# Optimization experiments

Measured on AMD Instinct MI355X. Metric: run time of the kernel, lower is better.

## Reference

```python
import jax, jax.numpy as jnp
import numpy as np

N_NODES = 100000
N_EDGES = 1600000
X_DIM, E_DIM = 4, 39


def setup_inputs() -> dict:
    key = jax.random.key(0)
    ks = jax.random.split(key, 12)
    x = jax.random.normal(ks[0], (N_NODES, X_DIM), dtype=jnp.float32)
    edge_index = jax.random.randint(ks[1], (2, N_EDGES), 0, N_NODES, dtype=jnp.int64)
    edge_attr = jax.random.normal(ks[2], (N_EDGES, E_DIM), dtype=jnp.float32)
    def lin(k, fan_in, fan_out):
        kw, kb = jax.random.split(k)
        bound = 1.0 / np.sqrt(fan_in)
        W = jax.random.uniform(kw, (fan_in, fan_out), jnp.float32, -bound, bound)
        b = jax.random.uniform(kb, (fan_out,), jnp.float32, -bound, bound)
        return W, b
    W1, b1 = lin(ks[3], 43, 64)
    W2, b2 = lin(ks[4], 64, 128)
    W3, b3 = lin(ks[5], 132, 256)
    W4, b4 = lin(ks[6], 256, 256)
    return {"x": x, "edge_index": edge_index, "edge_attr": edge_attr,
            "W1": W1, "b1": b1, "W2": W2, "b2": b2,
            "W3": W3, "b3": b3, "W4": W4, "b4": b4}


def reference(x, edge_index, edge_attr, W1, b1, W2, b2, W3, b3, W4, b4):
    row, col = edge_index[0], edge_index[1]
    n = x.shape[0]
    # gather source-node features, concat edge attrs -> edge MLP
    h = jnp.concatenate([x[col], edge_attr], axis=1)            # [E, 43]
    h = jax.nn.relu(h @ W1 + b1)                                # [E, 64]
    h = jax.nn.relu(h @ W2 + b2)                                # [E, 128]
    # scatter_mean over edges grouped by destination node `row`
    s = jax.ops.segment_sum(h, row, num_segments=n)             # [N, 128]
    cnt = jax.ops.segment_sum(jnp.ones((row.shape[0],), h.dtype), row,
                              num_segments=n)                   # [N]
    mean = s / jnp.maximum(cnt, 1.0)[:, None]                   # 0 for empty segments
    # concat node features with aggregated messages -> node MLP
    o = jnp.concatenate([x, mean], axis=1)                      # [N, 132]
    o = jax.nn.relu(o @ W3 + b3)                                # [N, 256]
    o = jax.nn.relu(o @ W4 + b4)                                # [N, 256]
    return o
```

## Files before the change

kernel.cpp:

```cpp
#include <hip/hip_runtime.h>
#include <hip/hip_bf16.h>

#define NN 100000
#define NE 1600000
#define XD 4
#define ED 39
#define K1 43
#define H1 64
#define H2 128
#define H3 256
#define NBN 16
#define NCHUNK 98

typedef short bfrag8 __attribute__((ext_vector_type(8)));
typedef float facc4  __attribute__((ext_vector_type(4)));
typedef unsigned short u16x4 __attribute__((ext_vector_type(4)));

static __device__ __forceinline__ unsigned short f2bf(float f) {
    __hip_bfloat16 b = __float2bfloat16(f);
    union { __hip_bfloat16 b; unsigned short u; } v; v.b = b;
    return v.u;
}
static __device__ __forceinline__ float bf2f(unsigned short h) {
    union { unsigned int u; float f; } v; v.u = ((unsigned int)h) << 16;
    return v.f;
}

__global__ __launch_bounds__(256) void hist_kernel(const int* __restrict__ eidx,
                                                   int* __restrict__ cnt,
                                                   int* __restrict__ rank) {
    int e = blockIdx.x * 256 + threadIdx.x;
    if (e < NE) rank[e] = atomicAdd(&cnt[eidx[e]], 1);
}

__global__ __launch_bounds__(1024) void scan1_kernel(const int* __restrict__ cnt,
                                                     int* __restrict__ row_ptr,
                                                     int* __restrict__ chunkSum) {
    __shared__ int wsum[16];
    const int t = threadIdx.x, lane = t & 63, w = t >> 6;
    const int i = blockIdx.x * 1024 + t;
    int v = (i < NN) ? cnt[i] : 0;
    int s = v;
    #pragma unroll
    for (int d = 1; d < 64; d <<= 1) {
        int u = __shfl_up(s, d, 64);
        if (lane >= d) s += u;
    }
    if (lane == 63) wsum[w] = s;
    __syncthreads();
    if (w == 0 && lane < 16) {
        int e = wsum[lane];
        #pragma unroll
        for (int d = 1; d < 16; d <<= 1) {
            int u = __shfl_up(e, d, 64);
            if (lane >= d) e += u;
        }
        wsum[lane] = e;
    }
    __syncthreads();
    int woff = (w == 0) ? 0 : wsum[w - 1];
    if (i < NN) row_ptr[i + 1] = woff + s;
    if (t == 0) chunkSum[blockIdx.x] = wsum[15];
}

__global__ __launch_bounds__(64) void scan2_kernel(const int* __restrict__ chunkSum,
                                                   int* __restrict__ chunkOff) {
    const int lane = threadIdx.x;
    int a = (lane < NCHUNK) ? chunkSum[lane] : 0;
    int b = (lane + 64 < NCHUNK) ? chunkSum[lane + 64] : 0;
    int sa = a;
    #pragma unroll
    for (int d = 1; d < 64; d <<= 1) {
        int u = __shfl_up(sa, d, 64);
        if (lane >= d) sa += u;
    }
    int totA = __shfl(sa, 63, 64);
    int sb = b;
    #pragma unroll
    for (int d = 1; d < 64; d <<= 1) {
        int u = __shfl_up(sb, d, 64);
        if (lane >= d) sb += u;
    }
    sb += totA;
    if (lane < NCHUNK) chunkOff[lane] = sa - a;
    if (lane + 64 < NCHUNK) chunkOff[lane + 64] = sb - b;
}

__global__ __launch_bounds__(1024) void scan3_kernel(const int* __restrict__ chunkOff,
                                                     int* __restrict__ row_ptr) {
    const int i = blockIdx.x * 1024 + threadIdx.x;
    const int off = chunkOff[blockIdx.x];
    if (i < NN) row_ptr[i + 1] += off;
    if (i == 0) row_ptr[0] = 0;
}

__global__ __launch_bounds__(256) void build_kernel(const int* __restrict__ eidx,
                                                    const int* __restrict__ row_ptr,
                                                    const int* __restrict__ rank,
                                                    int* __restrict__ perm) {
    int e = blockIdx.x * 256 + threadIdx.x;
    if (e < NE) {
        int r = eidx[e];
        perm[row_ptr[r] + rank[e]] = e;
    }
}

__global__ __launch_bounds__(256) void prep_kernel(
    const float* __restrict__ W1, const float* __restrict__ W2,
    const float* __restrict__ W3, const float* __restrict__ W4,
    unsigned short* __restrict__ W1h, unsigned short* __restrict__ W1l,
    unsigned short* __restrict__ W2h, unsigned short* __restrict__ W2l,
    unsigned short* __restrict__ W3h, unsigned short* __restrict__ W3l,
    unsigned short* __restrict__ W4h, unsigned short* __restrict__ W4l)
{
    int i = blockIdx.x * 256 + threadIdx.x;
    if (i >= 4096 + 8192 + 40960 + 65536) return;
    unsigned short *ph, *pl;
    int idx, col, k;
    float w;
    if (i < 4096) {
        idx = i;
        int grp = idx >> 9, lane = (idx >> 3) & 63, j = idx & 7;
        int wid = grp >> 1, ks = grp & 1;
        col = wid * 16 + (lane & 15);
        k   = ks * 32 + (lane >> 4) * 8 + j;
        w = (k < K1) ? W1[k * H1 + col] : 0.f;
        ph = W1h; pl = W1l;
    } else if (i < 12288) {
        idx = i - 4096;
        int grp = idx >> 9, lane = (idx >> 3) & 63, j = idx & 7;
        int wid = grp >> 2, nt = (grp >> 1) & 1, ks = grp & 1;
        col = wid * 32 + nt * 16 + (lane & 15);
        k   = ks * 32 + (lane >> 4) * 8 + j;
        w = W2[k * H2 + col];
        ph = W2h; pl = W2l;
    } else if (i < 53248) {
        idx = i - 12288;
        int grp = idx >> 9, lane = (idx >> 3) & 63, j = idx & 7;
        int w_ = grp / 20, rem = grp - w_ * 20;
        int ks = rem >> 2, nt = rem & 3;
        col = w_ * 64 + nt * 16 + (lane & 15);
        k   = ks * 32 + (lane >> 4) * 8 + j;
        w = (k < 132) ? W3[k * H3 + col] : 0.f;
        ph = W3h; pl = W3l;
    } else {
        idx = i - 53248;
        int grp = idx >> 9, lane = (idx >> 3) & 63, j = idx & 7;
        int w_ = grp >> 5, rem = grp & 31;
        int ks = rem >> 2, nt = rem & 3;
        col = w_ * 64 + nt * 16 + (lane & 15);
        k   = ks * 32 + (lane >> 4) * 8 + j;
        w = W4[k * H3 + col];
        ph = W4h; pl = W4l;
    }
    unsigned short h = f2bf(w);
    ph[idx] = h;
    pl[idx] = f2bf(w - bf2f(h));
}

__global__ __launch_bounds__(256, 3) void edge_agg_kernel(
    const float* __restrict__ x, const int* __restrict__ eidx,
    const float* __restrict__ ea,
    const unsigned short* __restrict__ W1h, const unsigned short* __restrict__ W1l,
    const float* __restrict__ b1,
    const unsigned short* __restrict__ W2h, const unsigned short* __restrict__ W2l,
    const float* __restrict__ b2,
    const unsigned short* __restrict__ W3h, const unsigned short* __restrict__ W3l,
    const float* __restrict__ b3,
    const unsigned short* __restrict__ W4h, const unsigned short* __restrict__ W4l,
    const float* __restrict__ b4,
    const int* __restrict__ row_ptr, const int* __restrict__ perm,
    float* __restrict__ out)
{
    __shared__ __align__(16) unsigned short uMem[4 * 64 * 72];
    __shared__ __align__(16) int sNode[72];
    __shared__ int sPerm[2][64], sCol[2][64], sRP[NBN + 1];

    unsigned short* Ahi   = uMem;
    unsigned short* Alo   = uMem + 64 * 72;
    unsigned short* H1hi  = uMem + 2 * 64 * 72;
    unsigned short* H1lo  = uMem + 3 * 64 * 72;
    unsigned short* H2Thi = uMem;
    unsigned short* H2Tlo = uMem + 128 * 72;
    unsigned short* nAh   = uMem;
    unsigned short* nAl   = uMem + 16 * 168;
    unsigned short* Hh    = uMem + 2 * 16 * 168;
    unsigned short* Hl    = uMem + 2 * 16 * 168 + 16 * 264;

    const int t    = threadIdx.x;
    const int lane = t & 63;
    const int wid  = t >> 6;
    const int cl   = lane & 15;
    const int lg   = lane >> 4;
    const int n0   = blockIdx.x * NBN;

    int p0 = -1, c0 = 0;
    if (t < 64) {
        int b0  = row_ptr[n0];
        int e0r = row_ptr[n0 + NBN];
        if (b0 + t < e0r) p0 = perm[b0 + t];
        if (p0 >= 0) c0 = eidx[NE + p0];
    }

    if (t <= NBN) sRP[t] = row_ptr[n0 + t];

    bfrag8 w1h_[2], w1l_[2], w2h_[2][2], w2l_[2][2];
    #pragma unroll
    for (int ks = 0; ks < 2; ks++) {
        const int off = ((wid * 2 + ks) * 64 + lane) * 8;
        w1h_[ks] = *(const bfrag8*)&W1h[off];
        w1l_[ks] = *(const bfrag8*)&W1l[off];
    }
    #pragma unroll
    for (int nt = 0; nt < 2; nt++)
        #pragma unroll
        for (int ks = 0; ks < 2; ks++) {
            const int off = (((wid * 2 + nt) * 2 + ks) * 64 + lane) * 8;
            w2h_[nt][ks] = *(const bfrag8*)&W2h[off];
            w2l_[nt][ks] = *(const bfrag8*)&W2l[off];
        }
    const float bias1 = b1[wid * 16 + cl];
    const float bias2[2] = { b2[wid * 32 + cl], b2[wid * 32 + 16 + cl] };

    facc4 acc_sel[2];
    #pragma unroll
    for (int nt = 0; nt < 2; nt++) {
        acc_sel[nt][0] = 0.f; acc_sel[nt][1] = 0.f;
        acc_sel[nt][2] = 0.f; acc_sel[nt][3] = 0.f;
    }

    if (t < 64) { sPerm[0][t] = p0; sCol[0][t] = c0; }
    __syncthreads();

    const int base = sRP[0], cntE = sRP[NBN] - base;

    auto loadA = [&](float (&pv)[4][4], const int* sP, const int* sC) {
        #pragma unroll
        for (int r = 0; r < 4; r++) {
            const int e  = (t >> 4) + r * 16;
            const int k0 = (t & 15) * 4;
            const int ee = sP[e];
            if (ee >= 0) {
                if (k0 == 0) {
                    float4 xv = *(const float4*)&x[(size_t)sC[e] * XD];
                    pv[r][0] = xv.x; pv[r][1] = xv.y; pv[r][2] = xv.z; pv[r][3] = xv.w;
                } else {
                    const float* er = ea + (size_t)ee * ED;
                    #pragma unroll
                    for (int q = 0; q < 4; q++) {
                        int k = k0 + q;
                        pv[r][q] = (k < K1) ? er[k - XD] : 0.f;
                    }
                }
            } else {
                pv[r][0] = pv[r][1] = pv[r][2] = pv[r][3] = 0.f;
            }
        }
    };

    if (cntE > 0) {
        float pv[4][4];
        loadA(pv, sPerm[0], sCol[0]);
        int buf = 0;

        for (int tb = 0; tb < cntE; tb += 64) {
            const int nv   = min(64, cntE - tb);
            const int nbuf = buf ^ 1;

            int pp = -1;
            if (t < 64 && tb + 64 < cntE)
                pp = (tb + 64 + t < cntE) ? perm[base + tb + 64 + t] : -1;

            #pragma unroll
            for (int r = 0; r < 4; r++) {
                const int e  = (t >> 4) + r * 16;
                const int k0 = (t & 15) * 4;
                u16x4 hv, lv;
                #pragma unroll
                for (int q = 0; q < 4; q++) {
                    unsigned short h = f2bf(pv[r][q]);
                    hv[q] = h;
                    lv[q] = f2bf(pv[r][q] - bf2f(h));
                }
                *(u16x4*)&Ahi[e * 72 + k0] = hv;
                *(u16x4*)&Alo[e * 72 + k0] = lv;
            }
            if (t < 72) {
                int nd = -1;
                if (t < nv) {
                    int idx = tb + t;
                    nd = 0;
                    #pragma unroll
                    for (int k = 1; k < 16; k++) nd += ((sRP[k] - base) <= idx);
                }
                sNode[t] = nd;
            }
            __syncthreads();

            int pc = 0;
            if (t < 64 && pp >= 0) pc = eidx[NE + pp];

            facc4 acc1[4];
            #pragma unroll
            for (int mt = 0; mt < 4; mt++) {
                acc1[mt][0] = bias1; acc1[mt][1] = bias1;
                acc1[mt][2] = bias1; acc1[mt][3] = bias1;
            }
            #pragma unroll
            for (int ks = 0; ks < 2; ks++) {
                #pragma unroll
                for (int mt = 0; mt < 4; mt++) {
                    const int ao = (mt * 16 + cl) * 72 + ks * 32 + lg * 8;
                    bfrag8 ah = *(const bfrag8*)&Ahi[ao];
                    bfrag8 al = *(const bfrag8*)&Alo[ao];
                    acc1[mt] = __builtin_amdgcn_mfma_f32_16x16x32_bf16(ah, w1h_[ks], acc1[mt], 0, 0, 0);
                    acc1[mt] = __builtin_amdgcn_mfma_f32_16x16x32_bf16(al, w1h_[ks], acc1[mt], 0, 0, 0);
                    acc1[mt] = __builtin_amdgcn_mfma_f32_16x16x32_bf16(ah, w1l_[ks], acc1[mt], 0, 0, 0);
                }
            }
            #pragma unroll
            for (int mt = 0; mt < 4; mt++)
                #pragma unroll
                for (int j = 0; j < 4; j++) {
                    float v = fmaxf(acc1[mt][j], 0.f);
                    unsigned short h = f2bf(v);
                    int m = mt * 16 + lg * 4 + j;
                    H1hi[m * 72 + wid * 16 + cl] = h;
                    H1lo[m * 72 + wid * 16 + cl] = f2bf(v - bf2f(h));
                }
            if (t < 64) { sPerm[nbuf][t] = pp; sCol[nbuf][t] = pc; }
            __syncthreads();

            if (tb + 64 < cntE) loadA(pv, sPerm[nbuf], sCol[nbuf]);

            facc4 acc2[4][2];
            #pragma unroll
            for (int mt = 0; mt < 4; mt++)
                #pragma unroll
                for (int nt = 0; nt < 2; nt++) {
                    acc2[mt][nt][0] = bias2[nt]; acc2[mt][nt][1] = bias2[nt];
                    acc2[mt][nt][2] = bias2[nt]; acc2[mt][nt][3] = bias2[nt];
                }
            #pragma unroll
            for (int ks = 0; ks < 2; ks++) {
                #pragma unroll
                for (int mt = 0; mt < 4; mt++) {
                    const int ao = (mt * 16 + cl) * 72 + ks * 32 + lg * 8;
                    bfrag8 ah = *(const bfrag8*)&H1hi[ao];
                    bfrag8 al = *(const bfrag8*)&H1lo[ao];
                    #pragma unroll
                    for (int nt = 0; nt < 2; nt++) {
                        acc2[mt][nt] = __builtin_amdgcn_mfma_f32_16x16x32_bf16(ah, w2h_[nt][ks], acc2[mt][nt], 0, 0, 0);
                        acc2[mt][nt] = __builtin_amdgcn_mfma_f32_16x16x32_bf16(al, w2h_[nt][ks], acc2[mt][nt], 0, 0, 0);
                        acc2[mt][nt] = __builtin_amdgcn_mfma_f32_16x16x32_bf16(ah, w2l_[nt][ks], acc2[mt][nt], 0, 0, 0);
                    }
                }
            }
            __syncthreads();

            #pragma unroll
            for (int mt = 0; mt < 4; mt++)
                #pragma unroll
                for (int nt = 0; nt < 2; nt++) {
                    const int c2 = wid * 32 + nt * 16 + cl;
                    u16x4 hv, lv;
                    #pragma unroll
                    for (int j = 0; j < 4; j++) {
                        float v = fmaxf(acc2[mt][nt][j], 0.f);
                        unsigned short h = f2bf(v);
                        hv[j] = h;
                        lv[j] = f2bf(v - bf2f(h));
                    }
                    const int eb = mt * 16 + lg * 4;
                    *(u16x4*)&H2Thi[c2 * 72 + eb] = hv;
                    *(u16x4*)&H2Tlo[c2 * 72 + eb] = lv;
                }
            __syncthreads();

            #pragma unroll
            for (int ks = 0; ks < 2; ks++) {
                const int4* np = (const int4*)&sNode[ks * 32 + lg * 8];
                int4 na = np[0], nb = np[1];
                bfrag8 sf;
                sf[0] = (na.x == cl) ? (short)0x3F80 : (short)0;
                sf[1] = (na.y == cl) ? (short)0x3F80 : (short)0;
                sf[2] = (na.z == cl) ? (short)0x3F80 : (short)0;
                sf[3] = (na.w == cl) ? (short)0x3F80 : (short)0;
                sf[4] = (nb.x == cl) ? (short)0x3F80 : (short)0;
                sf[5] = (nb.y == cl) ? (short)0x3F80 : (short)0;
                sf[6] = (nb.z == cl) ? (short)0x3F80 : (short)0;
                sf[7] = (nb.w == cl) ? (short)0x3F80 : (short)0;
                #pragma unroll
                for (int nt = 0; nt < 2; nt++) {
                    const int hb = (wid * 32 + nt * 16 + cl) * 72 + ks * 32 + lg * 8;
                    bfrag8 hh = *(const bfrag8*)&H2Thi[hb];
                    bfrag8 hl = *(const bfrag8*)&H2Tlo[hb];
                    acc_sel[nt] = __builtin_amdgcn_mfma_f32_16x16x32_bf16(sf, hh, acc_sel[nt], 0, 0, 0);
                    acc_sel[nt] = __builtin_amdgcn_mfma_f32_16x16x32_bf16(sf, hl, acc_sel[nt], 0, 0, 0);
                }
            }
            __syncthreads();
            buf = nbuf;
        }
    }

    __syncthreads();

    #pragma unroll
    for (int nt = 0; nt < 2; nt++)
        #pragma unroll
        for (int j = 0; j < 4; j++) {
            const int n = lg * 4 + j;
            const int deg = sRP[n + 1] - sRP[n];
            const float inv = (deg > 0) ? 1.f / (float)deg : 0.f;
            const float m = acc_sel[nt][j] * inv;
            unsigned short h = f2bf(m);
            const int k = 4 + wid * 32 + nt * 16 + cl;
            nAh[n * 168 + k] = h;
            nAl[n * 168 + k] = f2bf(m - bf2f(h));
        }
    if (t < 64) {
        const int n = t >> 2, k = t & 3;
        float xv = x[(size_t)(n0 + n) * XD + k];
        unsigned short h = f2bf(xv);
        nAh[n * 168 + k] = h;
        nAl[n * 168 + k] = f2bf(xv - bf2f(h));
    }
    for (int i = t; i < 448; i += 256) {
        int n = i / 28, k = 132 + (i - n * 28);
        nAh[n * 168 + k] = 0;
        nAl[n * 168 + k] = 0;
    }
    __syncthreads();

    facc4 na_[4];
    #pragma unroll
    for (int nt = 0; nt < 4; nt++) {
        float b = b3[wid * 64 + nt * 16 + cl];
        na_[nt][0] = b; na_[nt][1] = b; na_[nt][2] = b; na_[nt][3] = b;
    }
    #pragma unroll
    for (int ks = 0; ks < 5; ks++) {
        const int ao = cl * 168 + ks * 32 + lg * 8;
        bfrag8 ah = *(const bfrag8*)&nAh[ao];
        bfrag8 al = *(const bfrag8*)&nAl[ao];
        #pragma unroll
        for (int nt = 0; nt < 4; nt++) {
            const int wo = (((wid * 5 + ks) * 4 + nt) * 64 + lane) * 8;
            bfrag8 bh = *(const bfrag8*)&W3h[wo];
            bfrag8 bl = *(const bfrag8*)&W3l[wo];
            na_[nt] = __builtin_amdgcn_mfma_f32_16x16x32_bf16(ah, bh, na_[nt], 0, 0, 0);
            na_[nt] = __builtin_amdgcn_mfma_f32_16x16x32_bf16(al, bh, na_[nt], 0, 0, 0);
            na_[nt] = __builtin_amdgcn_mfma_f32_16x16x32_bf16(ah, bl, na_[nt], 0, 0, 0);
        }
    }
    #pragma unroll
    for (int nt = 0; nt < 4; nt++)
        #pragma unroll
        for (int j = 0; j < 4; j++) {
            float v = fmaxf(na_[nt][j], 0.f);
            const int r = lg * 4 + j;
            const int c = wid * 64 + nt * 16 + cl;
            unsigned short h = f2bf(v);
            Hh[r * 264 + c] = h;
            Hl[r * 264 + c] = f2bf(v - bf2f(h));
        }
    __syncthreads();

    facc4 nb_[4];
    #pragma unroll
    for (int nt = 0; nt < 4; nt++) {
        float b = b4[wid * 64 + nt * 16 + cl];
        nb_[nt][0] = b; nb_[nt][1] = b; nb_[nt][2] = b; nb_[nt][3] = b;
    }
    #pragma unroll
    for (int ks = 0; ks < 8; ks++) {
        const int ao = cl * 264 + ks * 32 + lg * 8;
        bfrag8 ah = *(const bfrag8*)&Hh[ao];
        bfrag8 al = *(const bfrag8*)&Hl[ao];
        #pragma unroll
        for (int nt = 0; nt < 4; nt++) {
            const int wo = (((wid * 8 + ks) * 4 + nt) * 64 + lane) * 8;
            bfrag8 bh = *(const bfrag8*)&W4h[wo];
            bfrag8 bl = *(const bfrag8*)&W4l[wo];
            nb_[nt] = __builtin_amdgcn_mfma_f32_16x16x32_bf16(ah, bh, nb_[nt], 0, 0, 0);
            nb_[nt] = __builtin_amdgcn_mfma_f32_16x16x32_bf16(al, bh, nb_[nt], 0, 0, 0);
            nb_[nt] = __builtin_amdgcn_mfma_f32_16x16x32_bf16(ah, bl, nb_[nt], 0, 0, 0);
        }
    }
    #pragma unroll
    for (int nt = 0; nt < 4; nt++)
        #pragma unroll
        for (int j = 0; j < 4; j++)
            out[(size_t)(n0 + lg * 4 + j) * H3 + wid * 64 + nt * 16 + cl] =
                fmaxf(nb_[nt][j], 0.f);
}

extern "C" void kernel_launch(void* const* d_in, const int* in_sizes, int n_in,
                              void* d_out, int out_size, void* d_ws, size_t ws_size,
                              hipStream_t stream) {
    const float* x    = (const float*)d_in[0];
    const int*   eidx = (const int*)  d_in[1];
    const float* ea   = (const float*)d_in[2];
    const float* W1   = (const float*)d_in[3];
    const float* b1   = (const float*)d_in[4];
    const float* W2   = (const float*)d_in[5];
    const float* b2   = (const float*)d_in[6];
    const float* W3   = (const float*)d_in[7];
    const float* b3   = (const float*)d_in[8];
    const float* W4   = (const float*)d_in[9];
    const float* b4   = (const float*)d_in[10];
    float* out = (float*)d_out;

    char* p = (char*)d_ws;
    int* perm     = (int*)p;  p += (size_t)NE * 4;
    int* rank     = (int*)p;  p += (size_t)NE * 4;
    int* row_ptr  = (int*)p;  p += ((size_t)NN + 8) * 4;
    int* cnt      = (int*)p;  p += (size_t)NN * 4;
    int* chunkSum = (int*)p;  p += 128 * 4;
    int* chunkOff = (int*)p;  p += 128 * 4;

    unsigned short* wp = (unsigned short*)rank;
    unsigned short* W1h_ = wp; wp += 64 * 64;
    unsigned short* W1l_ = wp; wp += 64 * 64;
    unsigned short* W2h_ = wp; wp += 128 * 64;
    unsigned short* W2l_ = wp; wp += 128 * 64;
    unsigned short* W3h_ = wp; wp += 256 * 160;
    unsigned short* W3l_ = wp; wp += 256 * 160;
    unsigned short* W4h_ = wp; wp += 256 * 256;
    unsigned short* W4l_ = wp; wp += 256 * 256;

    hipMemsetAsync(cnt, 0, (size_t)NN * 4, stream);

    hist_kernel <<<(NE + 255) / 256, 256, 0, stream>>>(eidx, cnt, rank);
    scan1_kernel<<<NCHUNK, 1024, 0, stream>>>(cnt, row_ptr, chunkSum);
    scan2_kernel<<<1, 64, 0, stream>>>(chunkSum, chunkOff);
    scan3_kernel<<<NCHUNK, 1024, 0, stream>>>(chunkOff, row_ptr);
    build_kernel<<<(NE + 255) / 256, 256, 0, stream>>>(eidx, row_ptr, rank, perm);
    prep_kernel <<<(4096 + 8192 + 40960 + 65536 + 255) / 256, 256, 0, stream>>>(
        W1, W2, W3, W4, W1h_, W1l_, W2h_, W2l_, W3h_, W3l_, W4h_, W4l_);
    edge_agg_kernel<<<NN / NBN, 256, 0, stream>>>(
        x, eidx, ea, W1h_, W1l_, b1, W2h_, W2l_, b2,
        W3h_, W3l_, b3, W4h_, W4l_, b4, row_ptr, perm, out);
}
```

Before: 778.4 us.

## Process 32 destination nodes per block to reuse node-MLP weights across two M-tiles

Doubles the nodes handled per block from 16 to 32. The segment-sum selector MFMA now produces two 16-node accumulator sets, and the node MLP (W3, W4) processes two M-tiles for each weight fragment loaded, halving weight traffic per node and halving the number of blocks. A barrier between writing H2T and the selector MFMA is removed, and shared buffers are reused with an extra sync. The costs are more accumulator registers and fewer blocks, which may reduce occupancy and load balance.

```diff
diff --git a/kernel.cpp b/kernel.cpp
--- a/kernel.cpp
+++ b/kernel.cpp
@@ -9,7 +9,7 @@
 #define H1 64
 #define H2 128
 #define H3 256
-#define NBN 16
+#define NBN 32
 #define NCHUNK 98
 
 typedef short bfrag8 __attribute__((ext_vector_type(8)));
@@ -173,7 +173,7 @@
     float* __restrict__ out)
 {
     __shared__ __align__(16) unsigned short uMem[4 * 64 * 72];
-    __shared__ __align__(16) int sNode[72];
+    __shared__ __align__(16) int sNode[64];
     __shared__ int sPerm[2][64], sCol[2][64], sRP[NBN + 1];
 
     unsigned short* Ahi   = uMem;
@@ -183,9 +183,9 @@
     unsigned short* H2Thi = uMem;
     unsigned short* H2Tlo = uMem + 128 * 72;
     unsigned short* nAh   = uMem;
-    unsigned short* nAl   = uMem + 16 * 168;
-    unsigned short* Hh    = uMem + 2 * 16 * 168;
-    unsigned short* Hl    = uMem + 2 * 16 * 168 + 16 * 264;
+    unsigned short* nAl   = uMem + 32 * 168;
+    unsigned short* Hh    = uMem;
+    unsigned short* Hl    = uMem + 32 * 264;
 
     const int t    = threadIdx.x;
     const int lane = t & 63;
@@ -222,12 +222,14 @@
     const float bias1 = b1[wid * 16 + cl];
     const float bias2[2] = { b2[wid * 32 + cl], b2[wid * 32 + 16 + cl] };
 
-    facc4 acc_sel[2];
-    #pragma unroll
-    for (int nt = 0; nt < 2; nt++) {
-        acc_sel[nt][0] = 0.f; acc_sel[nt][1] = 0.f;
-        acc_sel[nt][2] = 0.f; acc_sel[nt][3] = 0.f;
-    }
+    facc4 acc_sel[2][2];
+    #pragma unroll
+    for (int sg = 0; sg < 2; sg++)
+        #pragma unroll
+        for (int nt = 0; nt < 2; nt++) {
+            acc_sel[sg][nt][0] = 0.f; acc_sel[sg][nt][1] = 0.f;
+            acc_sel[sg][nt][2] = 0.f; acc_sel[sg][nt][3] = 0.f;
+        }
 
     if (t < 64) { sPerm[0][t] = p0; sCol[0][t] = c0; }
     __syncthreads();
@@ -285,13 +287,13 @@
                 *(u16x4*)&Ahi[e * 72 + k0] = hv;
                 *(u16x4*)&Alo[e * 72 + k0] = lv;
             }
-            if (t < 72) {
+            if (t < 64) {
                 int nd = -1;
                 if (t < nv) {
                     int idx = tb + t;
                     nd = 0;
                     #pragma unroll
-                    for (int k = 1; k < 16; k++) nd += ((sRP[k] - base) <= idx);
+                    for (int k = 1; k < NBN; k++) nd += ((sRP[k] - base) <= idx);
                 }
                 sNode[t] = nd;
             }
@@ -375,28 +377,37 @@
                     *(u16x4*)&H2Thi[c2 * 72 + eb] = hv;
                     *(u16x4*)&H2Tlo[c2 * 72 + eb] = lv;
                 }
-            __syncthreads();
 
             #pragma unroll
             for (int ks = 0; ks < 2; ks++) {
                 const int4* np = (const int4*)&sNode[ks * 32 + lg * 8];
                 int4 na = np[0], nb = np[1];
-                bfrag8 sf;
-                sf[0] = (na.x == cl) ? (short)0x3F80 : (short)0;
-                sf[1] = (na.y == cl) ? (short)0x3F80 : (short)0;
-                sf[2] = (na.z == cl) ? (short)0x3F80 : (short)0;
-                sf[3] = (na.w == cl) ? (short)0x3F80 : (short)0;
-                sf[4] = (nb.x == cl) ? (short)0x3F80 : (short)0;
-                sf[5] = (nb.y == cl) ? (short)0x3F80 : (short)0;
-                sf[6] = (nb.z == cl) ? (short)0x3F80 : (short)0;
-                sf[7] = (nb.w == cl) ? (short)0x3F80 : (short)0;
+                bfrag8 sf0, sf1;
+                sf0[0] = (na.x == cl)      ? (short)0x3F80 : (short)0;
+                sf0[1] = (na.y == cl)      ? (short)0x3F80 : (short)0;
+                sf0[2] = (na.z == cl)      ? (short)0x3F80 : (short)0;
+                sf0[3] = (na.w == cl)      ? (short)0x3F80 : (short)0;
+                sf0[4] = (nb.x == cl)      ? (short)0x3F80 : (short)0;
+                sf0[5] = (nb.y == cl)      ? (short)0x3F80 : (short)0;
+                sf0[6] = (nb.z == cl)      ? (short)0x3F80 : (short)0;
+                sf0[7] = (nb.w == cl)      ? (short)0x3F80 : (short)0;
+                sf1[0] = (na.x == cl + 16) ? (short)0x3F80 : (short)0;
+                sf1[1] = (na.y == cl + 16) ? (short)0x3F80 : (short)0;
+                sf1[2] = (na.z == cl + 16) ? (short)0x3F80 : (short)0;
+                sf1[3] = (na.w == cl + 16) ? (short)0x3F80 : (short)0;
+                sf1[4] = (nb.x == cl + 16) ? (short)0x3F80 : (short)0;
+                sf1[5] = (nb.y == cl + 16) ? (short)0x3F80 : (short)0;
+                sf1[6] = (nb.z == cl + 16) ? (short)0x3F80 : (short)0;
+                sf1[7] = (nb.w == cl + 16) ? (short)0x3F80 : (short)0;
                 #pragma unroll
                 for (int nt = 0; nt < 2; nt++) {
                     const int hb = (wid * 32 + nt * 16 + cl) * 72 + ks * 32 + lg * 8;
                     bfrag8 hh = *(const bfrag8*)&H2Thi[hb];
                     bfrag8 hl = *(const bfrag8*)&H2Tlo[hb];
-                    acc_sel[nt] = __builtin_amdgcn_mfma_f32_16x16x32_bf16(sf, hh, acc_sel[nt], 0, 0, 0);
-                    acc_sel[nt] = __builtin_amdgcn_mfma_f32_16x16x32_bf16(sf, hl, acc_sel[nt], 0, 0, 0);
+                    acc_sel[0][nt] = __builtin_amdgcn_mfma_f32_16x16x32_bf16(sf0, hh, acc_sel[0][nt], 0, 0, 0);
+                    acc_sel[0][nt] = __builtin_amdgcn_mfma_f32_16x16x32_bf16(sf0, hl, acc_sel[0][nt], 0, 0, 0);
+                    acc_sel[1][nt] = __builtin_amdgcn_mfma_f32_16x16x32_bf16(sf1, hh, acc_sel[1][nt], 0, 0, 0);
+                    acc_sel[1][nt] = __builtin_amdgcn_mfma_f32_16x16x32_bf16(sf1, hl, acc_sel[1][nt], 0, 0, 0);
                 }
             }
             __syncthreads();
@@ -407,93 +418,123 @@
     __syncthreads();
 
     #pragma unroll
-    for (int nt = 0; nt < 2; nt++)
-        #pragma unroll
-        for (int j = 0; j < 4; j++) {
-            const int n = lg * 4 + j;
-            const int deg = sRP[n + 1] - sRP[n];
-            const float inv = (deg > 0) ? 1.f / (float)deg : 0.f;
-            const float m = acc_sel[nt][j] * inv;
-            unsigned short h = f2bf(m);
-            const int k = 4 + wid * 32 + nt * 16 + cl;
-            nAh[n * 168 + k] = h;
-            nAl[n * 168 + k] = f2bf(m - bf2f(h));
-        }
-    if (t < 64) {
+    for (int sg = 0; sg < 2; sg++)
+        #pragma unroll
+        for (int nt = 0; nt < 2; nt++)
+            #pragma unroll
+            for (int j = 0; j < 4; j++) {
+                const int n = sg * 16 + lg * 4 + j;
+                const int deg = sRP[n + 1] - sRP[n];
+                const float inv = (deg > 0) ? 1.f / (float)deg : 0.f;
+                const float m = acc_sel[sg][nt][j] * inv;
+                unsigned short h = f2bf(m);
+                const int k = 4 + wid * 32 + nt * 16 + cl;
+                nAh[n * 168 + k] = h;
+                nAl[n * 168 + k] = f2bf(m - bf2f(h));
+            }
+    if (t < 128) {
         const int n = t >> 2, k = t & 3;
         float xv = x[(size_t)(n0 + n) * XD + k];
         unsigned short h = f2bf(xv);
         nAh[n * 168 + k] = h;
         nAl[n * 168 + k] = f2bf(xv - bf2f(h));
     }
-    for (int i = t; i < 448; i += 256) {
+    for (int i = t; i < 896; i += 256) {
         int n = i / 28, k = 132 + (i - n * 28);
         nAh[n * 168 + k] = 0;
         nAl[n * 168 + k] = 0;
     }
     __syncthreads();
 
-    facc4 na_[4];
+    facc4 na_[2][4];
     #pragma unroll
     for (int nt = 0; nt < 4; nt++) {
         float b = b3[wid * 64 + nt * 16 + cl];
-        na_[nt][0] = b; na_[nt][1] = b; na_[nt][2] = b; na_[nt][3] = b;
+        #pragma unroll
+        for (int mt = 0; mt < 2; mt++) {
+            na_[mt][nt][0] = b; na_[mt][nt][1] = b;
+            na_[mt][nt][2] = b; na_[mt][nt][3] = b;
+        }
     }
     #pragma unroll
     for (int ks = 0; ks < 5; ks++) {
-        const int ao = cl * 168 + ks * 32 + lg * 8;
-        bfrag8 ah = *(const bfrag8*)&nAh[ao];
-        bfrag8 al = *(const bfrag8*)&nAl[ao];
+        bfrag8 ah[2], al[2];
+        #pragma unroll
+        for (int mt = 0; mt < 2; mt++) {
+            const int ao = (mt * 16 + cl) * 168 + ks * 32 + lg * 8;
+            ah[mt] = *(const bfrag8*)&nAh[ao];
+            al[mt] = *(const bfrag8*)&nAl[ao];
+        }
         #pragma unroll
         for (int nt = 0; nt < 4; nt++) {
             const int wo = (((wid * 5 + ks) * 4 + nt) * 64 + lane) * 8;
             bfrag8 bh = *(const bfrag8*)&W3h[wo];
             bfrag8 bl = *(const bfrag8*)&W3l[wo];
-            na_[nt] = __builtin_amdgcn_mfma_f32_16x16x32_bf16(ah, bh, na_[nt], 0, 0, 0);
-            na_[nt] = __builtin_amdgcn_mfma_f32_16x16x32_bf16(al, bh, na_[nt], 0, 0, 0);
-            na_[nt] = __builtin_amdgcn_mfma_f32_16x16x32_bf16(ah, bl, na_[nt], 0, 0, 0);
-        }
-    }
-    #pragma unroll
-    for (int nt = 0; nt < 4; nt++)
-        #pragma unroll
-        for (int j = 0; j < 4; j++) {
-            float v = fmaxf(na_[nt][j], 0.f);
-            const int r = lg * 4 + j;
-            const int c = wid * 64 + nt * 16 + cl;
-            unsigned short h = f2bf(v);
-            Hh[r * 264 + c] = h;
-            Hl[r * 264 + c] = f2bf(v - bf2f(h));
-        }
-    __syncthreads();
-
-    facc4 nb_[4];
+            #pragma unroll
+            for (int mt = 0; mt < 2; mt++) {
+                na_[mt][nt] = __builtin_amdgcn_mfma_f32_16x16x32_bf16(ah[mt], bh, na_[mt][nt], 0, 0, 0);
+                na_[mt][nt] = __builtin_amdgcn_mfma_f32_16x16x32_bf16(al[mt], bh, na_[mt][nt], 0, 0, 0);
+                na_[mt][nt] = __builtin_amdgcn_mfma_f32_16x16x32_bf16(ah[mt], bl, na_[mt][nt], 0, 0, 0);
+            }
+        }
+    }
+    __syncthreads();
+
+    #pragma unroll
+    for (int mt = 0; mt < 2; mt++)
+        #pragma unroll
+        for (int nt = 0; nt < 4; nt++)
+            #pragma unroll
+            for (int j = 0; j < 4; j++) {
+                float v = fmaxf(na_[mt][nt][j], 0.f);
+                const int r = mt * 16 + lg * 4 + j;
+                const int c = wid * 64 + nt * 16 + cl;
+                unsigned short h = f2bf(v);
+                Hh[r * 264 + c] = h;
+                Hl[r * 264 + c] = f2bf(v - bf2f(h));
+            }
+    __syncthreads();
+
+    facc4 nb_[2][4];
     #pragma unroll
     for (int nt = 0; nt < 4; nt++) {
         float b = b4[wid * 64 + nt * 16 + cl];
-        nb_[nt][0] = b; nb_[nt][1] = b; nb_[nt][2] = b; nb_[nt][3] = b;
+        #pragma unroll
+        for (int mt = 0; mt < 2; mt++) {
+            nb_[mt][nt][0] = b; nb_[mt][nt][1] = b;
+            nb_[mt][nt][2] = b; nb_[mt][nt][3] = b;
+        }
     }
     #pragma unroll
     for (int ks = 0; ks < 8; ks++) {
-        const int ao = cl * 264 + ks * 32 + lg * 8;
-        bfrag8 ah = *(const bfrag8*)&Hh[ao];
-        bfrag8 al = *(const bfrag8*)&Hl[ao];
+        bfrag8 ah[2], al[2];
+        #pragma unroll
+        for (int mt = 0; mt < 2; mt++) {
+            const int ao = (mt * 16 + cl) * 264 + ks * 32 + lg * 8;
+            ah[mt] = *(const bfrag8*)&Hh[ao];
+            al[mt] = *(const bfrag8*)&Hl[ao];
+        }
         #pragma unroll
         for (int nt = 0; nt < 4; nt++) {
             const int wo = (((wid * 8 + ks) * 4 + nt) * 64 + lane) * 8;
             bfrag8 bh = *(const bfrag8*)&W4h[wo];
             bfrag8 bl = *(const bfrag8*)&W4l[wo];
-            nb_[nt] = __builtin_amdgcn_mfma_f32_16x16x32_bf16(ah, bh, nb_[nt], 0, 0, 0);
-            nb_[nt] = __builtin_amdgcn_mfma_f32_16x16x32_bf16(al, bh, nb_[nt], 0, 0, 0);
-            nb_[nt] = __builtin_amdgcn_mfma_f32_16x16x32_bf16(ah, bl, nb_[nt], 0, 0, 0);
-        }
-    }
-    #pragma unroll
-    for (int nt = 0; nt < 4; nt++)
-        #pragma unroll
-        for (int j = 0; j < 4; j++)
-            out[(size_t)(n0 + lg * 4 + j) * H3 + wid * 64 + nt * 16 + cl] =
-                fmaxf(nb_[nt][j], 0.f);
+            #pragma unroll
+            for (int mt = 0; mt < 2; mt++) {
+                nb_[mt][nt] = __builtin_amdgcn_mfma_f32_16x16x32_bf16(ah[mt], bh, nb_[mt][nt], 0, 0, 0);
+                nb_[mt][nt] = __builtin_amdgcn_mfma_f32_16x16x32_bf16(al[mt], bh, nb_[mt][nt], 0, 0, 0);
+                nb_[mt][nt] = __builtin_amdgcn_mfma_f32_16x16x32_bf16(ah[mt], bl, nb_[mt][nt], 0, 0, 0);
+            }
+        }
+    }
+    #pragma unroll
+    for (int mt = 0; mt < 2; mt++)
+        #pragma unroll
+        for (int nt = 0; nt < 4; nt++)
+            #pragma unroll
+            for (int j = 0; j < 4; j++)
+                out[(size_t)(n0 + mt * 16 + lg * 4 + j) * H3 + wid * 64 + nt * 16 + cl] =
+                    fmaxf(nb_[mt][nt][j], 0.f);
 }
 
 extern "C" void kernel_launch(void* const* d_in, const int* in_sizes, int n_in,
```

Result: slower. 818.8 us (+5.2%).
